# Performance work log

Measured on AMD Instinct MI355X. Metric: run time of the kernel, lower is better.

## Reference

```python
import jax, jax.numpy as jnp
import numpy as np

INPUT_DIM, OUTPUT_DIM = 128, 256
FPS_FACTOR, KNN = 14, 10


def fps(pcd, K):
    """Farthest point sampling. pcd: [B,N,3] -> (points [B,K,3], indices [B,K]).
    Deterministic start at index 0 (pytorch3d uses first/random point)."""
    B, N, _ = pcd.shape
    first = jnp.zeros((B,), jnp.int32)
    init_d = jnp.full((B, N), 1e10, pcd.dtype)

    def step(carry, _):
        dists, last = carry
        lp = jnp.take_along_axis(pcd, last[:, None, None], axis=1)  # [B,1,3]
        d = jnp.sum((pcd - lp) ** 2, axis=-1)                        # [B,N]
        dists = jnp.minimum(dists, d)
        nxt = jnp.argmax(dists, axis=-1).astype(jnp.int32)
        return (dists, nxt), nxt

    (_, _), rest = jax.lax.scan(step, (init_d, first), None, length=K - 1)
    idx = jnp.concatenate([first[None, :], rest], axis=0).T  # [B,K]
    pts = jnp.take_along_axis(pcd, idx[..., None], axis=1)   # [B,K,3]
    return pts, idx


def knn_idx(q, p, k):
    """q:[B,Q,3], p:[B,N,3] -> nearest-neighbor indices [B,Q,k] (squared L2)."""
    d = (jnp.sum(q * q, -1)[:, :, None] + jnp.sum(p * p, -1)[:, None, :]
         - 2.0 * jnp.einsum('bqc,bnc->bqn', q, p))
    _, idx = jax.lax.top_k(-d, k)
    return idx


_bgather = jax.vmap(lambda a, i: a[i])  # per-batch fancy gather


def setup_inputs() -> dict:
    key = jax.random.key(0)
    k1, k2, k3, k4, k5 = jax.random.split(key, 5)
    B, N = 4, 16384
    tgt = jax.random.normal(k1, (B, N, INPUT_DIM), jnp.float32)
    pcd_x = jax.random.normal(k2, (B, N, 3), jnp.float32)
    pcd_v = jax.random.normal(k3, (B, N, 3, 3), jnp.float32)
    W = jax.random.normal(k4, (INPUT_DIM, OUTPUT_DIM), jnp.float32) / np.sqrt(INPUT_DIM)
    b = jax.random.normal(k5, (OUTPUT_DIM,), jnp.float32) * 0.01
    return {"tgt": tgt, "pcd_x": pcd_x, "pcd_v": pcd_v, "W": W, "b": b}


def reference(tgt, pcd_x, pcd_v, W, b):
    B, N, D = tgt.shape
    n_out = N // FPS_FACTOR
    out_pcd_x, out_indices = fps(pcd_x, n_out)          # [B,n_out,3], [B,n_out]
    nn = knn_idx(out_pcd_x, pcd_x, KNN)                 # [B,n_out,k]

    knn_pcd = _bgather(pcd_x, nn)                       # [B,n_out,k,3]
    query_f = jnp.take_along_axis(tgt, out_indices[..., None], axis=1)  # [B,n_out,D]
    query_c = out_pcd_x
    query_v = _bgather(pcd_v, out_indices)              # [B,n_out,V,3]
    key_f = _bgather(tgt, nn)                           # [B,n_out,k,D]
    key_c = knn_pcd
    key_v = _bgather(pcd_v, nn)                         # [B,n_out,k,V,3]

    # flatten (B*n_out) super-point groups, project features
    _query_f = query_f.reshape(-1, D)[:, None, :] @ W + b          # [B*n_out,1,O]
    _key_f = key_f.reshape(-1, KNN, D) @ W + b                     # [B*n_out,k,O]
    del _key_f, key_c, key_v  # consumed by the (identity stand-in) transformer

    # NOTE: URSATransformer stand-in = identity on the projected query features
    out_query_f = _query_f.reshape(B, n_out, OUTPUT_DIM)
    return out_query_f, query_c, query_v
```

## Files before the change

kernel.cpp:

```cpp
#include <hip/hip_runtime.h>

constexpr int B_   = 4;
constexpr int N_   = 16384;
constexpr int NOUT = 1170;
constexpr int D_   = 128;
constexpr int O_   = 256;

typedef float f32x2 __attribute__((ext_vector_type(2)));
typedef unsigned long long u64;

template <int CTRL>
__device__ __forceinline__ float dpp_fmax(float x) {
  int yi = __builtin_amdgcn_update_dpp(__float_as_int(x), __float_as_int(x),
                                       CTRL, 0xF, 0xF, false);
  return fmaxf(x, __int_as_float(yi));
}

constexpr int TPB_FPS = 1024;
constexpr int NPR   = 8;
constexpr int NW    = TPB_FPS / 64;
constexpr size_t LDS_BYTES = (size_t)2 * N_ * 4 + NW * 4 + 16;

__global__ __launch_bounds__(TPB_FPS, 1)
void fps_kernel(const float* __restrict__ pcd_x,
                int* __restrict__ sel,
                float* __restrict__ out_c) {
  extern __shared__ char smem_raw[];
  f32x2*  xs2   = (f32x2*)smem_raw;
  f32x2*  ys2   = xs2 + 8 * 1024;
  float*  s_val = (float*)(ys2 + 8 * 1024);
  float4* s_res = (float4*)(s_val + NW);

  const int b = blockIdx.x, t = threadIdx.x;
  const int lane = t & 63, w = t >> 6;
  const float* __restrict__ P = pcd_x + (size_t)b * N_ * 3;

  f32x2 zs[NPR], dm[NPR];
#pragma unroll
  for (int h = 0; h < NPR; ++h) {
    const int p0 = 16 * t + 2 * h;
    xs2[h * 1024 + t] = f32x2{P[p0 * 3 + 0], P[p0 * 3 + 3]};
    ys2[h * 1024 + t] = f32x2{P[p0 * 3 + 1], P[p0 * 3 + 4]};
    zs[h] = f32x2{P[p0 * 3 + 2], P[p0 * 3 + 5]};
    dm[h] = f32x2{1e10f, 1e10f};
  }
  __syncthreads();

  float lx = P[0], ly = P[1], lz = P[2];
  if (t == 0) {
    sel[b * NOUT + 0] = 0;
    out_c[((size_t)b * NOUT + 0) * 3 + 0] = lx;
    out_c[((size_t)b * NOUT + 0) * 3 + 1] = ly;
    out_c[((size_t)b * NOUT + 0) * 3 + 2] = lz;
  }

  for (int step = 1; step < NOUT; ++step) {
    const float nx = __int_as_float(__float_as_int(lx) ^ 0x80000000);
    const float ny = __int_as_float(__float_as_int(ly) ^ 0x80000000);
    const float nz = __int_as_float(__float_as_int(lz) ^ 0x80000000);
    const f32x2 nlx = {nx, nx}, nly = {ny, ny}, nlz = {nz, nz};

    f32x2 bvv = {-1.0f, -1.0f};
    {
#pragma clang fp contract(off)
#pragma unroll
      for (int h = 0; h < NPR; ++h) {
        const f32x2 xv = xs2[h * 1024 + t];
        const f32x2 yv = ys2[h * 1024 + t];
        const f32x2 dx = xv + nlx;
        const f32x2 dy = yv + nly;
        const f32x2 dz = zs[h] + nlz;
        const f32x2 s  = (dx * dx + dy * dy) + dz * dz;
        dm[h] = __builtin_elementwise_min(dm[h], s);
        bvv   = __builtin_elementwise_max(bvv, dm[h]);
      }
    }
    const float bv = fmaxf(bvv.x, bvv.y);

    asm volatile("" : "+v"(zs[0]), "+v"(zs[1]), "+v"(zs[2]), "+v"(zs[3]),
                      "+v"(zs[4]), "+v"(zs[5]), "+v"(zs[6]), "+v"(zs[7]));
    asm volatile("" : "+v"(dm[0]), "+v"(dm[1]), "+v"(dm[2]), "+v"(dm[3]),
                      "+v"(dm[4]), "+v"(dm[5]), "+v"(dm[6]), "+v"(dm[7]));

    float wm = bv;
    wm = dpp_fmax<0xB1>(wm);
    wm = dpp_fmax<0x4E>(wm);
    wm = dpp_fmax<0x141>(wm);
    wm = dpp_fmax<0x140>(wm);
    wm = dpp_fmax<0x142>(wm);
    wm = dpp_fmax<0x143>(wm);
    const float wmax =
        __int_as_float(__builtin_amdgcn_readlane(__float_as_int(wm), 63));
    if (lane == 0) s_val[w] = wmax;
    __syncthreads();

    const float e = s_val[lane & (NW - 1)];
    float gv = e;
    gv = dpp_fmax<0xB1>(gv);
    gv = dpp_fmax<0x4E>(gv);
    gv = dpp_fmax<0x141>(gv);
    gv = dpp_fmax<0x140>(gv);

    const u64 wwm = __ballot((lane < NW) && (e == gv));
    const int ww = __builtin_ctzll(wwm);

    if (w == ww && bv == gv) {
      const u64 am = __ballot(true);
      if (lane == __builtin_ctzll(am)) {
        int bi = 0;
#pragma unroll
        for (int h = NPR - 1; h >= 0; --h) {
          if (dm[h].y == bv) bi = 16 * t + 2 * h + 1;
          if (dm[h].x == bv) bi = 16 * t + 2 * h;
        }
        const int loc = bi & 15, hh = loc >> 1, hf = loc & 1;
        const f32x2 xv = xs2[hh * 1024 + t];
        const f32x2 yv = ys2[hh * 1024 + t];
        const float wx = hf ? xv.y : xv.x;
        const float wy = hf ? yv.y : yv.x;
        const float wz = hf ? zs[hh].y : zs[hh].x;
        s_res[0] = make_float4(wx, wy, wz, __int_as_float(bi));
        sel[b * NOUT + step] = bi;
        out_c[((size_t)b * NOUT + step) * 3 + 0] = wx;
        out_c[((size_t)b * NOUT + step) * 3 + 1] = wy;
        out_c[((size_t)b * NOUT + step) * 3 + 2] = wz;
      }
    }
    __syncthreads();

    const float4 r = s_res[0];
    lx = r.x; ly = r.y; lz = r.z;
  }
}

constexpr int TPB_PROJ = 256;
constexpr int RPB = 4;

__global__ __launch_bounds__(TPB_PROJ)
void proj_kernel(const float* __restrict__ tgt,
                 const float* __restrict__ pcd_v,
                 const float* __restrict__ W,
                 const float* __restrict__ bias,
                 const int* __restrict__ sel,
                 float* __restrict__ out_f,
                 float* __restrict__ out_v) {
  const int t = threadIdx.x;
  const int row0 = blockIdx.x * RPB;
  __shared__ float sA[RPB * D_];
  __shared__ int   sIdx[RPB];
  if (t < RPB) {
    const int row = row0 + t;
    const int b = row / NOUT;
    sIdx[t] = b * N_ + sel[row];
  }
  __syncthreads();
#pragma unroll
  for (int l = 0; l < RPB * D_ / TPB_PROJ; ++l) {
    const int e = t + l * TPB_PROJ;
    const int r = e >> 7, k = e & (D_ - 1);
    sA[e] = tgt[(size_t)sIdx[r] * D_ + k];
  }
  __syncthreads();
  float acc0 = 0.f, acc1 = 0.f, acc2 = 0.f, acc3 = 0.f;
#pragma unroll 8
  for (int k = 0; k < D_; ++k) {
    const float w = W[k * O_ + t];
    acc0 = fmaf(sA[0 * D_ + k], w, acc0);
    acc1 = fmaf(sA[1 * D_ + k], w, acc1);
    acc2 = fmaf(sA[2 * D_ + k], w, acc2);
    acc3 = fmaf(sA[3 * D_ + k], w, acc3);
  }
  const float bb = bias[t];
  out_f[(size_t)(row0 + 0) * O_ + t] = acc0 + bb;
  out_f[(size_t)(row0 + 1) * O_ + t] = acc1 + bb;
  out_f[(size_t)(row0 + 2) * O_ + t] = acc2 + bb;
  out_f[(size_t)(row0 + 3) * O_ + t] = acc3 + bb;
  if (t < RPB * 9) {
    const int r = t / 9, e = t - r * 9;
    out_v[(size_t)(row0 + r) * 9 + e] = pcd_v[(size_t)sIdx[r] * 9 + e];
  }
}

extern "C" void kernel_launch(void* const* d_in, const int* in_sizes, int n_in,
                              void* d_out, int out_size, void* d_ws, size_t ws_size,
                              hipStream_t stream) {
  const float* tgt   = (const float*)d_in[0];
  const float* pcd_x = (const float*)d_in[1];
  const float* pcd_v = (const float*)d_in[2];
  const float* W     = (const float*)d_in[3];
  const float* bias  = (const float*)d_in[4];

  float* out   = (float*)d_out;
  float* out_f = out;
  float* out_c = out + (size_t)B_ * NOUT * O_;
  float* out_v = out_c + (size_t)B_ * NOUT * 3;

  int* sel = (int*)d_ws;

  hipLaunchKernelGGL(fps_kernel, dim3(B_), dim3(TPB_FPS), LDS_BYTES, stream,
                     pcd_x, sel, out_c);
  hipLaunchKernelGGL(proj_kernel, dim3(B_ * NOUT / RPB), dim3(TPB_PROJ), 0, stream,
                     tgt, pcd_v, W, bias, sel, out_f, out_v);
}
```

Before: 1.975 ms.

## Keep FPS x/y coordinates in AGPRs and store interleaved xy in LDS

Per-thread x and y coordinates are moved out of LDS and into accumulation registers (AGPRs) through inline asm. The hot distance loop now reads them with v_accvgpr_read instead of LDS loads. LDS keeps one interleaved xy copy indexed by point id. All threads fetch the winner's x/y from it after the barrier, and thread 0 writes the output coordinates. This takes LDS traffic off the serial per-step critical path, at the cost of extra accvgpr read instructions and a broadcast LDS read after the sync.

```diff
diff --git a/kernel.cpp b/kernel.cpp
--- a/kernel.cpp
+++ b/kernel.cpp
@@ -16,32 +16,41 @@
   return fmaxf(x, __int_as_float(yi));
 }
 
+#define AWRITE(dst, src) \
+  asm volatile("v_accvgpr_write_b32 %0, %1" : "=a"(dst) : "v"(src))
+#define AREAD(dst, src) \
+  asm volatile("v_accvgpr_read_b32 %0, %1" : "=v"(dst) : "a"(src))
+
 constexpr int TPB_FPS = 1024;
 constexpr int NPR   = 8;
 constexpr int NW    = TPB_FPS / 64;
-constexpr size_t LDS_BYTES = (size_t)2 * N_ * 4 + NW * 4 + 16;
+constexpr size_t LDS_BYTES = (size_t)N_ * 8 + NW * 4 + 16;
 
 __global__ __launch_bounds__(TPB_FPS, 1)
 void fps_kernel(const float* __restrict__ pcd_x,
                 int* __restrict__ sel,
                 float* __restrict__ out_c) {
   extern __shared__ char smem_raw[];
-  f32x2*  xs2   = (f32x2*)smem_raw;
-  f32x2*  ys2   = xs2 + 8 * 1024;
-  float*  s_val = (float*)(ys2 + 8 * 1024);
-  float4* s_res = (float4*)(s_val + NW);
+  f32x2*  xy    = (f32x2*)smem_raw;
+  float*  s_val = (float*)(xy + N_);
+  float2* s_res = (float2*)(s_val + NW);
 
   const int b = blockIdx.x, t = threadIdx.x;
   const int lane = t & 63, w = t >> 6;
   const float* __restrict__ P = pcd_x + (size_t)b * N_ * 3;
 
+  float ax[2 * NPR], ay[2 * NPR];
   f32x2 zs[NPR], dm[NPR];
 #pragma unroll
   for (int h = 0; h < NPR; ++h) {
     const int p0 = 16 * t + 2 * h;
-    xs2[h * 1024 + t] = f32x2{P[p0 * 3 + 0], P[p0 * 3 + 3]};
-    ys2[h * 1024 + t] = f32x2{P[p0 * 3 + 1], P[p0 * 3 + 4]};
-    zs[h] = f32x2{P[p0 * 3 + 2], P[p0 * 3 + 5]};
+    const float x0 = P[p0 * 3 + 0], y0 = P[p0 * 3 + 1], z0 = P[p0 * 3 + 2];
+    const float x1 = P[p0 * 3 + 3], y1 = P[p0 * 3 + 4], z1 = P[p0 * 3 + 5];
+    xy[p0]     = f32x2{x0, y0};
+    xy[p0 + 1] = f32x2{x1, y1};
+    AWRITE(ax[2 * h], x0);  AWRITE(ax[2 * h + 1], x1);
+    AWRITE(ay[2 * h], y0);  AWRITE(ay[2 * h + 1], y1);
+    zs[h] = f32x2{z0, z1};
     dm[h] = f32x2{1e10f, 1e10f};
   }
   __syncthreads();
@@ -65,8 +74,11 @@
 #pragma clang fp contract(off)
 #pragma unroll
       for (int h = 0; h < NPR; ++h) {
-        const f32x2 xv = xs2[h * 1024 + t];
-        const f32x2 yv = ys2[h * 1024 + t];
+        float xl, xh, yl, yh;
+        AREAD(xl, ax[2 * h]);  AREAD(xh, ax[2 * h + 1]);
+        AREAD(yl, ay[2 * h]);  AREAD(yh, ay[2 * h + 1]);
+        const f32x2 xv = {xl, xh};
+        const f32x2 yv = {yl, yh};
         const f32x2 dx = xv + nlx;
         const f32x2 dy = yv + nly;
         const f32x2 dz = zs[h] + nlz;
@@ -114,22 +126,22 @@
           if (dm[h].x == bv) bi = 16 * t + 2 * h;
         }
         const int loc = bi & 15, hh = loc >> 1, hf = loc & 1;
-        const f32x2 xv = xs2[hh * 1024 + t];
-        const f32x2 yv = ys2[hh * 1024 + t];
-        const float wx = hf ? xv.y : xv.x;
-        const float wy = hf ? yv.y : yv.x;
         const float wz = hf ? zs[hh].y : zs[hh].x;
-        s_res[0] = make_float4(wx, wy, wz, __int_as_float(bi));
+        s_res[0] = make_float2(wz, __int_as_float(bi));
         sel[b * NOUT + step] = bi;
-        out_c[((size_t)b * NOUT + step) * 3 + 0] = wx;
-        out_c[((size_t)b * NOUT + step) * 3 + 1] = wy;
-        out_c[((size_t)b * NOUT + step) * 3 + 2] = wz;
       }
     }
     __syncthreads();
 
-    const float4 r = s_res[0];
-    lx = r.x; ly = r.y; lz = r.z;
+    const float2 r = s_res[0];
+    const int ri = __float_as_int(r.y);
+    const f32x2 xyv = xy[ri];
+    lx = xyv.x; ly = xyv.y; lz = r.x;
+    if (t == 0) {
+      out_c[((size_t)b * NOUT + step) * 3 + 0] = lx;
+      out_c[((size_t)b * NOUT + step) * 3 + 1] = ly;
+      out_c[((size_t)b * NOUT + step) * 3 + 2] = lz;
+    }
   }
 }
 
```

After: 1.995 ms. About the same (+1.0%).
